# Optimization experiments

Hardware: AMD Instinct MI355X
Metric: run time of the kernel (lower is better)

## Reference

```python
import jax, jax.numpy as jnp
import numpy as np

POOL = (7, 7)
A = -0.5  # Keys cubic coefficient, matches TF v2 tf.image.resize(method='bicubic')


def _cubic_weights(t):
    # t in [0,1); weights for taps at floor-1, floor, floor+1, floor+2
    t2 = t * t
    t3 = t2 * t
    wm1 = A * (t3 - 2.0 * t2 + t)
    w0 = (A + 2.0) * t3 - (A + 3.0) * t2 + 1.0
    u = 1.0 - t
    w1 = (A + 2.0) * u * u * u - (A + 3.0) * u * u + 1.0
    w2 = A * (t2 - t3)
    return jnp.stack([wm1, w0, w1, w2], axis=-1)


def _axis_taps(lo, hi, out_size, max_idx):
    # lo/hi: [B,N] integer-valued pixel crop bounds (hi exclusive).
    # Returns tap indices [B,N,out,4] int32 and cubic weights [B,N,out,4].
    span = hi - lo
    grid = (jnp.arange(out_size, dtype=jnp.float32) + 0.5) / out_size
    s = lo[..., None] + grid * span[..., None] - 0.5  # half-pixel centers
    f = jnp.floor(s)
    t = s - f
    idx = f[..., None] + jnp.arange(-1.0, 3.0)
    lo_c = lo[..., None, None]
    hi_c = jnp.maximum(hi[..., None, None] - 1.0, lo_c)
    idx = jnp.clip(jnp.clip(idx, lo_c, hi_c), 0.0, max_idx).astype(jnp.int32)
    return idx, _cubic_weights(t)


def _pool_level(fm, py1, px1, py2, px2):
    # fm: [B,H,W,C]; bounds: [B,N]. Returns [B,N,ph,pw,C].
    B, H, W, C = fm.shape
    iy, wy = _axis_taps(py1, py2, POOL[0], H - 1)  # [B,N,ph,4]
    ix, wx = _axis_taps(px1, px2, POOL[1], W - 1)  # [B,N,pw,4]
    bi = jnp.arange(B).reshape(B, 1, 1, 1, 1, 1)
    # gather the 4x4 bicubic neighborhood: [B,N,ph,pw,4,4,C]
    vals = fm[bi, iy[:, :, :, None, :, None], ix[:, :, None, :, None, :]]
    return jnp.einsum('bnik,bnjl,bnijklc->bnijc', wy, wx, vals)


def _forward(boxes, image_shape, feature_maps):
    y1, x1, y2, x2 = [boxes[..., k] for k in range(4)]
    h = y2 - y1
    w = x2 - x1
    area = (image_shape[0] * image_shape[1]).astype(jnp.float32)
    roi = jnp.log2(jnp.sqrt(h * w) / (224.0 / jnp.sqrt(area)))
    roi_level = jnp.clip(4 + jnp.round(roi).astype(jnp.int32), 2, 5)  # [B,N]
    B, N = boxes.shape[:2]
    C = feature_maps[0].shape[-1]
    out = jnp.zeros((B, N, POOL[0], POOL[1], C), dtype=feature_maps[0].dtype)
    for level, fm in zip((2, 3, 4, 5), feature_maps):
        H, W = fm.shape[1], fm.shape[2]
        scale = jnp.array([H, W, H, W], dtype=jnp.float32)
        b = jax.lax.stop_gradient(jnp.round(boxes * scale))  # denorm_box
        py1 = jnp.minimum(b[..., 0], b[..., 2])
        px1 = jnp.minimum(b[..., 1], b[..., 3])
        py2 = jnp.maximum(b[..., 0], b[..., 2])
        px2 = jnp.maximum(b[..., 1], b[..., 3])
        pooled = _pool_level(fm, py1, px1, py2, px2)
        # zero-sum denormed boxes produce zeros (per original), and only boxes
        # routed to this level contribute; final gather/sort restores original
        # box order, which masked accumulation reproduces directly.
        valid = (roi_level == level) & ((py1 + px1 + py2 + px2) != 0.0)
        out = out + pooled * valid[..., None, None, None].astype(out.dtype)
    return out


def setup_inputs() -> dict:
    key = jax.random.key(0)
    ks = jax.random.split(key, 9)
    B, N, C = 2, 200, 256
    y1 = jax.random.uniform(ks[0], (B, N)) * 0.6
    x1 = jax.random.uniform(ks[1], (B, N)) * 0.6
    hh = 0.05 + jax.random.uniform(ks[2], (B, N)) * 0.35
    ww = 0.05 + jax.random.uniform(ks[3], (B, N)) * 0.35
    boxes = jnp.stack([y1, x1, jnp.minimum(y1 + hh, 1.0), jnp.minimum(x1 + ww, 1.0)], axis=-1)
    return {
        'boxes': boxes.astype(jnp.float32),
        'image_shape': jnp.array([1024, 1024, 3], dtype=jnp.int32),
        'p2': jax.random.normal(ks[4], (B, 256, 256, C), dtype=jnp.float32),
        'p3': jax.random.normal(ks[5], (B, 128, 128, C), dtype=jnp.float32),
        'p4': jax.random.normal(ks[6], (B, 64, 64, C), dtype=jnp.float32),
        'p5': jax.random.normal(ks[7], (B, 32, 32, C), dtype=jnp.float32),
    }


def reference(boxes, image_shape, p2, p3, p4, p5):
    return _forward(boxes, image_shape, (p2, p3, p4, p5))
```

## Files before the change

kernel.cpp:

```cpp
#include <hip/hip_runtime.h>

constexpr int POOL = 7;
constexpr int NC = 256;

__global__ __launch_bounds__(256)
void roi_align_kernel(const float* __restrict__ boxes,
                      const int*   __restrict__ ishape,
                      const float* __restrict__ p2,
                      const float* __restrict__ p3,
                      const float* __restrict__ p4,
                      const float* __restrict__ p5,
                      float*       __restrict__ out,
                      int B, int N)
{
    int tid  = blockIdx.x * 256 + threadIdx.x;
    int c4   = tid & 63;
    int cell = tid >> 6;
    if (cell >= B * N * POOL * POOL) return;

    int j = cell % POOL;
    int i = (cell / POOL) % POOL;
    int n = (cell / (POOL * POOL)) % N;
    int b = cell / (POOL * POOL * N);

    const float* bp = boxes + 4 * (b * N + n);
    float y1 = bp[0], x1 = bp[1], y2 = bp[2], x2 = bp[3];

    float area  = (float)(ishape[0] * ishape[1]);
    float denom = 224.0f / sqrtf(area);
    float roi   = log2f(sqrtf((y2 - y1) * (x2 - x1)) / denom);
    int lvl = 4 + (int)rintf(roi);
    lvl = lvl < 2 ? 2 : (lvl > 5 ? 5 : lvl);

    const float* fm; int H;
    if      (lvl == 2) { fm = p2; H = 256; }
    else if (lvl == 3) { fm = p3; H = 128; }
    else if (lvl == 4) { fm = p4; H = 64;  }
    else               { fm = p5; H = 32;  }
    const int W = H;
    const float Hf = (float)H, Wf = (float)W;

    float by1 = rintf(y1 * Hf), bx1 = rintf(x1 * Wf);
    float by2 = rintf(y2 * Hf), bx2 = rintf(x2 * Wf);
    float py1 = fminf(by1, by2), px1 = fminf(bx1, bx2);
    float py2 = fmaxf(by1, by2), px2 = fmaxf(bx1, bx2);

    float* op = out + (size_t)cell * NC + (size_t)c4 * 4;

    if (py1 + px1 + py2 + px2 == 0.0f) {
        float4 z = {0.f, 0.f, 0.f, 0.f};
        *(float4*)op = z;
        return;
    }

    const float A = -0.5f;

    int iy[4]; float wy[4];
    {
        float span = py2 - py1;
        float grid = ((float)i + 0.5f) / (float)POOL;
        float s = py1 + grid * span - 0.5f;
        float f = floorf(s);
        float t = s - f;
        float hi_c = fmaxf(py2 - 1.0f, py1);
        float maxi = Hf - 1.0f;
        #pragma unroll
        for (int k = 0; k < 4; ++k) {
            float idx = f + (float)(k - 1);
            idx = fminf(fmaxf(idx, py1), hi_c);
            idx = fminf(fmaxf(idx, 0.0f), maxi);
            iy[k] = (int)idx;
        }
        float t2 = t * t, t3 = t2 * t;
        float u = 1.0f - t, u2 = u * u, u3 = u2 * u;
        wy[0] = A * (t3 - 2.0f * t2 + t);
        wy[1] = (A + 2.0f) * t3 - (A + 3.0f) * t2 + 1.0f;
        wy[2] = (A + 2.0f) * u3 - (A + 3.0f) * u2 + 1.0f;
        wy[3] = A * (t2 - t3);
    }

    int ix[4]; float wx[4];
    {
        float span = px2 - px1;
        float grid = ((float)j + 0.5f) / (float)POOL;
        float s = px1 + grid * span - 0.5f;
        float f = floorf(s);
        float t = s - f;
        float hi_c = fmaxf(px2 - 1.0f, px1);
        float maxi = Wf - 1.0f;
        #pragma unroll
        for (int l = 0; l < 4; ++l) {
            float idx = f + (float)(l - 1);
            idx = fminf(fmaxf(idx, px1), hi_c);
            idx = fminf(fmaxf(idx, 0.0f), maxi);
            ix[l] = (int)idx;
        }
        float t2 = t * t, t3 = t2 * t;
        float u = 1.0f - t, u2 = u * u, u3 = u2 * u;
        wx[0] = A * (t3 - 2.0f * t2 + t);
        wx[1] = (A + 2.0f) * t3 - (A + 3.0f) * t2 + 1.0f;
        wx[2] = (A + 2.0f) * u3 - (A + 3.0f) * u2 + 1.0f;
        wx[3] = A * (t2 - t3);
    }

    float4 acc = {0.f, 0.f, 0.f, 0.f};
    const size_t chan_off = (size_t)c4 * 4;
    const size_t bbase = (size_t)b * H * W * NC + chan_off;
    #pragma unroll
    for (int k = 0; k < 4; ++k) {
        const float* row = fm + bbase + (size_t)iy[k] * (size_t)(W * NC);
        #pragma unroll
        for (int l = 0; l < 4; ++l) {
            float wgt = wy[k] * wx[l];
            float4 v = *(const float4*)(row + (size_t)ix[l] * NC);
            acc.x += wgt * v.x;
            acc.y += wgt * v.y;
            acc.z += wgt * v.z;
            acc.w += wgt * v.w;
        }
    }
    *(float4*)op = acc;
}

extern "C" void kernel_launch(void* const* d_in, const int* in_sizes, int n_in,
                              void* d_out, int out_size, void* d_ws, size_t ws_size,
                              hipStream_t stream) {
    const float* boxes  = (const float*)d_in[0];
    const int*   ishape = (const int*)d_in[1];
    const float* p2     = (const float*)d_in[2];
    const float* p3     = (const float*)d_in[3];
    const float* p4     = (const float*)d_in[4];
    const float* p5     = (const float*)d_in[5];
    float* out = (float*)d_out;

    int B = in_sizes[2] / (256 * 256 * 256);
    int N = in_sizes[0] / (4 * B);

    int total_threads = B * N * POOL * POOL * 64;
    int blocks = (total_threads + 255) / 256;
    roi_align_kernel<<<blocks, 256, 0, stream>>>(boxes, ishape, p2, p3, p4, p5, out, B, N);
}
```

Baseline: 211.6 us.

## Separate bicubic interpolation into vertical pass over row span and horizontal pass via LDS

```diff
diff --git a/kernel.cpp b/kernel.cpp
--- a/kernel.cpp
+++ b/kernel.cpp
@@ -2,26 +2,25 @@
 
 constexpr int POOL = 7;
 constexpr int NC = 256;
+constexpr int CHUNK = 32;
 
 __global__ __launch_bounds__(256)
-void roi_align_kernel(const float* __restrict__ boxes,
-                      const int*   __restrict__ ishape,
-                      const float* __restrict__ p2,
-                      const float* __restrict__ p3,
-                      const float* __restrict__ p4,
-                      const float* __restrict__ p5,
-                      float*       __restrict__ out,
-                      int B, int N)
+void roi_align_row_kernel(const float* __restrict__ boxes,
+                          const int*   __restrict__ ishape,
+                          const float* __restrict__ p2,
+                          const float* __restrict__ p3,
+                          const float* __restrict__ p4,
+                          const float* __restrict__ p5,
+                          float*       __restrict__ out,
+                          int B, int N)
 {
-    int tid  = blockIdx.x * 256 + threadIdx.x;
-    int c4   = tid & 63;
-    int cell = tid >> 6;
-    if (cell >= B * N * POOL * POOL) return;
+    __shared__ float vy[CHUNK][NC];
 
-    int j = cell % POOL;
-    int i = (cell / POOL) % POOL;
-    int n = (cell / (POOL * POOL)) % N;
-    int b = cell / (POOL * POOL * N);
+    int blk = blockIdx.x;
+    int i = blk % POOL;
+    int n = (blk / POOL) % N;
+    int b = blk / (POOL * N);
+    int c = threadIdx.x;
 
     const float* bp = boxes + 4 * (b * N + n);
     float y1 = bp[0], x1 = bp[1], y2 = bp[2], x2 = bp[3];
@@ -45,11 +44,11 @@
     float py1 = fminf(by1, by2), px1 = fminf(bx1, bx2);
     float py2 = fmaxf(by1, by2), px2 = fmaxf(bx1, bx2);
 
-    float* op = out + (size_t)cell * NC + (size_t)c4 * 4;
+    size_t obase = (size_t)blk * POOL * NC + (size_t)c;
 
     if (py1 + px1 + py2 + px2 == 0.0f) {
-        float4 z = {0.f, 0.f, 0.f, 0.f};
-        *(float4*)op = z;
+        #pragma unroll
+        for (int j = 0; j < POOL; ++j) out[obase + (size_t)j * NC] = 0.0f;
         return;
     }
 
@@ -79,47 +78,74 @@
         wy[3] = A * (t2 - t3);
     }
 
-    int ix[4]; float wx[4];
+    int   ix[POOL][4];
+    float wx[POOL][4];
     {
         float span = px2 - px1;
-        float grid = ((float)j + 0.5f) / (float)POOL;
-        float s = px1 + grid * span - 0.5f;
-        float f = floorf(s);
-        float t = s - f;
         float hi_c = fmaxf(px2 - 1.0f, px1);
         float maxi = Wf - 1.0f;
         #pragma unroll
-        for (int l = 0; l < 4; ++l) {
-            float idx = f + (float)(l - 1);
-            idx = fminf(fmaxf(idx, px1), hi_c);
-            idx = fminf(fmaxf(idx, 0.0f), maxi);
-            ix[l] = (int)idx;
+        for (int j = 0; j < POOL; ++j) {
+            float grid = ((float)j + 0.5f) / (float)POOL;
+            float s = px1 + grid * span - 0.5f;
+            float f = floorf(s);
+            float t = s - f;
+            #pragma unroll
+            for (int l = 0; l < 4; ++l) {
+                float idx = f + (float)(l - 1);
+                idx = fminf(fmaxf(idx, px1), hi_c);
+                idx = fminf(fmaxf(idx, 0.0f), maxi);
+                ix[j][l] = (int)idx;
+            }
+            float t2 = t * t, t3 = t2 * t;
+            float u = 1.0f - t, u2 = u * u, u3 = u2 * u;
+            wx[j][0] = A * (t3 - 2.0f * t2 + t);
+            wx[j][1] = (A + 2.0f) * t3 - (A + 3.0f) * t2 + 1.0f;
+            wx[j][2] = (A + 2.0f) * u3 - (A + 3.0f) * u2 + 1.0f;
+            wx[j][3] = A * (t2 - t3);
         }
-        float t2 = t * t, t3 = t2 * t;
-        float u = 1.0f - t, u2 = u * u, u3 = u2 * u;
-        wx[0] = A * (t3 - 2.0f * t2 + t);
-        wx[1] = (A + 2.0f) * t3 - (A + 3.0f) * t2 + 1.0f;
-        wx[2] = (A + 2.0f) * u3 - (A + 3.0f) * u2 + 1.0f;
-        wx[3] = A * (t2 - t3);
     }
 
-    float4 acc = {0.f, 0.f, 0.f, 0.f};
-    const size_t chan_off = (size_t)c4 * 4;
-    const size_t bbase = (size_t)b * H * W * NC + chan_off;
+    int x_lo = ix[0][0];
+    int x_hi = ix[POOL - 1][3];
+
+    const float* row0 = fm + ((size_t)b * H + iy[0]) * (size_t)(W * NC) + c;
+    const float* row1 = fm + ((size_t)b * H + iy[1]) * (size_t)(W * NC) + c;
+    const float* row2 = fm + ((size_t)b * H + iy[2]) * (size_t)(W * NC) + c;
+    const float* row3 = fm + ((size_t)b * H + iy[3]) * (size_t)(W * NC) + c;
+
+    float acc[POOL];
     #pragma unroll
-    for (int k = 0; k < 4; ++k) {
-        const float* row = fm + bbase + (size_t)iy[k] * (size_t)(W * NC);
+    for (int j = 0; j < POOL; ++j) acc[j] = 0.0f;
+
+    for (int x0 = x_lo; x0 <= x_hi; x0 += CHUNK) {
+        int xe = x0 + CHUNK - 1;
+        if (xe > x_hi) xe = x_hi;
+
+        if (x0 > x_lo) __syncthreads();
+
+        for (int x = x0; x <= xe; ++x) {
+            size_t o = (size_t)x * NC;
+            float v = wy[0] * row0[o] + wy[1] * row1[o]
+                    + wy[2] * row2[o] + wy[3] * row3[o];
+            vy[x - x0][c] = v;
+        }
+        __syncthreads();
+
         #pragma unroll
-        for (int l = 0; l < 4; ++l) {
-            float wgt = wy[k] * wx[l];
-            float4 v = *(const float4*)(row + (size_t)ix[l] * NC);
-            acc.x += wgt * v.x;
-            acc.y += wgt * v.y;
-            acc.z += wgt * v.z;
-            acc.w += wgt * v.w;
+        for (int j = 0; j < POOL; ++j) {
+            #pragma unroll
+            for (int l = 0; l < 4; ++l) {
+                int xr = ix[j][l] - x0;
+                if (xr >= 0 && xr <= xe - x0)
+                    acc[j] += wx[j][l] * vy[xr][c];
+            }
         }
     }
-    *(float4*)op = acc;
+
+    #pragma unroll
+    for (int j = 0; j < POOL; ++j)
+        out[obase + (size_t)j * NC] = acc[j];
 }
 
 extern "C" void kernel_launch(void* const* d_in, const int* in_sizes, int n_in,
@@ -136,7 +162,6 @@
     int B = in_sizes[2] / (256 * 256 * 256);
     int N = in_sizes[0] / (4 * B);
 
-    int total_threads = B * N * POOL * POOL * 64;
-    int blocks = (total_threads + 255) / 256;
-    roi_align_kernel<<<blocks, 256, 0, stream>>>(boxes, ishape, p2, p3, p4, p5, out, B, N);
+    int blocks = B * N * POOL;
+    roi_align_row_kernel<<<blocks, 256, 0, stream>>>(boxes, ishape, p2, p3, p4, p5, out, B, N);
 }
```

Result: slower. 241.0 us (+13.9%).
